# Kernel optimization log

Measured on AMD Instinct MI355X. Metric: run time of the kernel, lower is better.

## Reference

```python
import jax, jax.numpy as jnp
import numpy as np

EPS = 1e-12


def pairwise_sqdist(x, y):
    # x: (B, N, 3), y: (B, M, 3) -> (B, N, M) squared euclidean distances
    xx = jnp.sum(x * x, axis=-1)              # (B, N)
    yy = jnp.sum(y * y, axis=-1)              # (B, M)
    xy = jnp.einsum('bnd,bmd->bnm', x, y)     # (B, N, M)
    d = xx[:, :, None] + yy[None_ if False else yy[:, None, :].shape and 0 or ...] if False else xx[:, :, None] + yy[:, None, :] - 2.0 * xy
    return jnp.maximum(d, 0.0)


def chamfer_l1(x, y):
    # pytorch3d/PoinTr-style ChamferDistanceL1:
    # mean over points of sqrt(min squared dist), averaged over both directions
    d = pairwise_sqdist(x, y)                 # (B, N, M)
    d1 = jnp.min(d, axis=2)                   # (B, N) x -> nearest y
    d2 = jnp.min(d, axis=1)                   # (B, M) y -> nearest x
    d1 = jnp.sqrt(jnp.maximum(d1, EPS))
    d2 = jnp.sqrt(jnp.maximum(d2, EPS))
    return 0.5 * (jnp.mean(d1) + jnp.mean(d2))


def knn1_gather(x, y):
    # For each point in x (B,N,3), find nearest neighbor in y (B,M,3) (K=1)
    # and gather it -> (B, N, 3). Matches knn_points + knn_gather + squeeze.
    d = pairwise_sqdist(x, y)                 # (B, N, M)
    idx = jnp.argmin(d, axis=2)               # (B, N) int
    return jnp.take_along_axis(y, idx[:, :, None], axis=1)  # (B, N, 3)


def volume_with_wedge(p):
    # wedge-product volume over consecutive point triples:
    # V = sum_i (p_i x p_{i+1}) . p_{i+2} / 6  -> (B,)
    c = jnp.cross(p[:, :-2, :], p[:, 1:-1, :])  # (B, N-2, 3)
    return jnp.sum(jnp.einsum('bnd,bnd->bn', c, p[:, 2:, :]), axis=-1) / 6.0


def setup_inputs() -> dict:
    key = jax.random.key(0)
    k1, k2, k3 = jax.random.split(key, 3)
    B, Nc, Nf, M = 2, 512, 8192, 8192
    return {
        'source_coarse': jax.random.normal(k1, (B, Nc, 3), dtype=jnp.float32),
        'source_fine': jax.random.normal(k2, (B, Nf, 3), dtype=jnp.float32),
        'target_points': jax.random.normal(k3, (B, M, 3), dtype=jnp.float32),
    }


def reference(source_coarse, source_fine, target_points):
    lambda_rot = lambda_ref = lambda_align = lambda_geo = 1.0
    B = source_fine.shape[0]
    axis = jnp.broadcast_to(jnp.array([0.0, 0.0, 1.0], dtype=source_fine.dtype), (B, 3))
    plane_normal = jnp.broadcast_to(jnp.array([0.0, 1.0, 0.0], dtype=source_fine.dtype), (B, 3))

    # KNN (K=1) gather of nearest target point for each fine source point
    new_target = knn1_gather(source_fine, target_points)  # (B, Nf, 3)

    # alignment (Chamfer L1) losses
    loss_align_coarse = chamfer_l1(source_coarse, target_points)
    loss_align_fine = chamfer_l1(source_fine, target_points)

    # rotational symmetry loss
    in_proj = jnp.einsum('bij,bj->bi', source_fine, axis)      # (B, Nf)
    re_proj = jnp.einsum('bij,bj->bi', new_target, axis)
    loss_rot = jnp.mean((jnp.linalg.norm(in_proj, axis=-1) - jnp.linalg.norm(re_proj, axis=-1)) ** 2)

    # reflectional symmetry loss
    pn = plane_normal / jnp.linalg.norm(plane_normal, axis=-1, keepdims=True)
    in_dist = jnp.einsum('bij,bj->bi', source_fine, pn)
    re_dist = jnp.einsum('bij,bj->bi', new_target, pn)
    loss_ref = jnp.mean((in_dist - re_dist) ** 2)

    # geometric consistency (wedge-product volume) loss
    loss_geo = jnp.mean((volume_with_wedge(source_fine) - volume_with_wedge(new_target)) ** 2)

    total = (lambda_rot * loss_rot + lambda_ref * loss_ref
             + lambda_align * loss_align_coarse + lambda_align * loss_align_fine
             + lambda_geo * loss_geo)
    return total
```

## Files before the change

### kernel.cpp

```cpp
#include <hip/hip_runtime.h>
#include <stdint.h>
#include <float.h>

using u64 = unsigned long long;
typedef float v2f __attribute__((ext_vector_type(2)));

constexpr int B_ = 2;
constexpr int NC = 512;
constexpr int NF = 8192;
constexpr int MT = 8192;

constexpr int TPB = 256;
constexpr int CF  = 16;
constexpr int TAIL_BLOCKS = 196;

#define DEVINL __device__ __forceinline__

DEVINL v2f pk_mul_vs(v2f a, v2f b){ v2f d; asm("v_pk_mul_f32 %0, %1, %2" : "=v"(d) : "v"(a), "s"(b)); return d; }
DEVINL v2f pk_add_vv(v2f a, v2f b){ v2f d; asm("v_pk_add_f32 %0, %1, %2" : "=v"(d) : "v"(a), "v"(b)); return d; }
DEVINL v2f pk_add_vs(v2f a, v2f b){ v2f d; asm("v_pk_add_f32 %0, %1, %2" : "=v"(d) : "v"(a), "s"(b)); return d; }

__global__ __launch_bounds__(TPB) void prep(
    const float* __restrict__ coarse, const float* __restrict__ fine,
    const float* __restrict__ tgt,
    float* __restrict__ finep, float* __restrict__ tgtp,
    float* __restrict__ coarsep, unsigned* __restrict__ counter)
{
#pragma clang fp contract(off)
    int g = blockIdx.x * TPB + threadIdx.x;
    if (g == 0) *counter = 0;
    if (g < B_ * NF / 2) {
        {
            const float* p = fine + (size_t)g * 6;
            float x0=p[0],y0=p[1],z0=p[2],x1=p[3],y1=p[4],z1=p[5];
            float* o = finep + (size_t)g * 8;
            o[0]=x0; o[1]=x1; o[2]=y0; o[3]=y1; o[4]=z0; o[5]=z1;
            o[6]=(x0*x0+y0*y0)+z0*z0;  o[7]=(x1*x1+y1*y1)+z1*z1;
        }
        {
            const float* p = tgt + (size_t)g * 6;
            float x0=p[0],y0=p[1],z0=p[2],x1=p[3],y1=p[4],z1=p[5];
            float* o = tgtp + (size_t)g * 8;
            o[0]=x0; o[1]=x1; o[2]=y0; o[3]=y1; o[4]=z0; o[5]=z1;
            o[6]=(x0*x0+y0*y0)+z0*z0;  o[7]=(x1*x1+y1*y1)+z1*z1;
        }
        if (g < B_ * NC / 2) {
            const float* p = coarse + (size_t)g * 6;
            float x0=p[0],y0=p[1],z0=p[2],x1=p[3],y1=p[4],z1=p[5];
            float* o = coarsep + (size_t)g * 8;
            o[0]=x0; o[1]=x1; o[2]=y0; o[3]=y1; o[4]=z0; o[5]=z1;
            o[6]=(x0*x0+y0*y0)+z0*z0;  o[7]=(x1*x1+y1*y1)+z1*z1;
        }
    }
}

template<bool ARGMIN>
DEVINL void pairmin_body(const float* __restrict__ P, const v2f* __restrict__ Qp,
                         int nP, int nQpairsB, int b, int row_base,
                         int jp0, int jplen, int chunk, int nRowsTot,
                         u64* __restrict__ outPack, unsigned* __restrict__ outVal)
{
#pragma clang fp contract(off)
    const int tid = threadIdx.x;
    const int row = row_base + tid;
    const float* p = P + ((size_t)b * nP + row) * 3;
    float a0 = p[0], a1 = p[1], a2 = p[2];
    v2f vax = {-2.0f * a0, -2.0f * a0};
    v2f vay = {-2.0f * a1, -2.0f * a1};
    v2f vaz = {-2.0f * a2, -2.0f * a2};
    float xx = (a0*a0 + a1*a1) + a2*a2;
    v2f vxx = {xx, xx};
    float db0 = FLT_MAX, db1 = FLT_MAX;
    int jb0 = 0, jb1 = 0;

    const v2f* Q = Qp + ((size_t)b * nQpairsB + jp0) * 4;
    v2f qx = Q[0], qy = Q[1], qz = Q[2], qw = Q[3];
    int j = jp0 * 2;
    for (int k = 0; k < jplen; ++k) {
        const v2f* Qn = Q + (size_t)(k + 1) * 4;
        v2f nx = Qn[0], ny = Qn[1], nz = Qn[2], nw = Qn[3];
        v2f m0  = pk_mul_vs(vax, qx);
        v2f m1  = pk_mul_vs(vay, qy);
        v2f m2  = pk_mul_vs(vaz, qz);
        v2f s01 = pk_add_vv(m0, m1);
        v2f sxy = pk_add_vv(s01, m2);
        v2f tt  = pk_add_vs(vxx, qw);
        v2f d   = pk_add_vv(tt, sxy);
        if (ARGMIN) {
            float c0 = fmaxf(d.x, 0.0f);
            float c1 = fmaxf(d.y, 0.0f);
            bool t0 = c0 < db0;  db0 = t0 ? c0 : db0;  jb0 = t0 ? j     : jb0;
            bool t1 = c1 < db1;  db1 = t1 ? c1 : db1;  jb1 = t1 ? (j+1) : jb1;
        } else {
            db0 = __builtin_amdgcn_fmed3f(d.x, 0.0f, db0);
            db1 = __builtin_amdgcn_fmed3f(d.y, 0.0f, db1);
        }
        qx = nx; qy = ny; qz = nz; qw = nw;
        j += 2;
    }
    const size_t o = (size_t)chunk * nRowsTot + (size_t)b * nP + row;
    if (ARGMIN) {
        bool odd = (db1 < db0) || (db1 == db0 && jb1 < jb0);
        float db = odd ? db1 : db0;
        int   jb = odd ? jb1 : jb0;
        outPack[o] = ((u64)__float_as_uint(db) << 32) | (unsigned)jb;
    } else {
        outVal[o] = __float_as_uint(fminf(db0, db1));
    }
}

__global__ __launch_bounds__(TPB, 8) void pairmin_all(
    const float* __restrict__ coarse, const float* __restrict__ fine,
    const float* __restrict__ tgt,
    const v2f* __restrict__ finep, const v2f* __restrict__ tgtp,
    const v2f* __restrict__ coarsep,
    u64* __restrict__ pfr, unsigned* __restrict__ pfc,
    unsigned* __restrict__ pcr, unsigned* __restrict__ pcc)
{
    const int bx = blockIdx.x;
    if (bx < 1024) {
        int chunk = bx & 15, yb = (bx >> 4) & 31, b = bx >> 9;
        pairmin_body<false>(tgt, finep, MT, NF/2, b, yb*TPB, chunk*256, 256,
                            chunk, B_*MT, nullptr, pfc);
    } else if (bx < 2048) {
        int i = bx - 1024;
        int chunk = i & 15, yb = (i >> 4) & 31, b = i >> 9;
        pairmin_body<true>(fine, tgtp, NF, MT/2, b, yb*TPB, chunk*256, 256,
                           chunk, B_*NF, pfr, nullptr);
    } else if (bx < 2112) {
        int i = bx - 2048;
        int chunk = i & 15, yb = (i >> 4) & 1, b = i >> 5;
        pairmin_body<false>(coarse, tgtp, NC, MT/2, b, yb*TPB, chunk*256, 256,
                            chunk, B_*NC, nullptr, pcr);
    } else {
        int i = bx - 2112;
        int yb = i & 31, b = i >> 5;
        pairmin_body<false>(tgt, coarsep, MT, NC/2, b, yb*TPB, 0, 256,
                            0, B_*MT, nullptr, pcc);
    }
}

__global__ __launch_bounds__(TPB) void tail_all(
    const float* __restrict__ fine, const float* __restrict__ tgt,
    const u64* __restrict__ pfr, const unsigned* __restrict__ pfc,
    const unsigned* __restrict__ pcr, const unsigned* __restrict__ pcc,
    double* __restrict__ bs, unsigned* __restrict__ counter,
    float* __restrict__ out)
{
    __shared__ float sp[TPB + 2][3], yp[TPB + 2][3];
    __shared__ double redw[4][9];
    __shared__ double lred[4][13];
    __shared__ int lastflag;
    const int bx = blockIdx.x, tid = threadIdx.x;
    const int wave = tid >> 6, lane = tid & 63;

    double v_s = 0, v_d2f = 0, v_d1c = 0, v_d2c = 0, v_yd2 = 0, v_zs = 0, v_zt = 0;
    double vs = 0, vt = 0;
    int role_b = 0;

    if (bx < 64) {
        const int base = bx * TPB;
        const int g = base + tid;
        const int b = base >> 13;  role_b = b;
        u64 best = pfr[g];
        #pragma unroll
        for (int c = 1; c < CF; ++c) {
            u64 p = pfr[(size_t)c * (B_ * NF) + g];
            best = p < best ? p : best;
        }
        float d1 = __uint_as_float((unsigned)(best >> 32));
        int idx  = (int)(best & 0xffffffffULL);
        float s = sqrtf(fmaxf(d1, 1e-12f));
        const float* y  = tgt  + ((size_t)b * MT + idx) * 3;
        const float* sr = fine + (size_t)g * 3;
        float y0 = y[0],  y1 = y[1],  y2 = y[2];
        float s0 = sr[0], s1 = sr[1], s2 = sr[2];
        yp[tid][0] = y0; yp[tid][1] = y1; yp[tid][2] = y2;
        sp[tid][0] = s0; sp[tid][1] = s1; sp[tid][2] = s2;
        const int base_b = base & (NF - 1);
        if (tid < 2 && base_b + TPB + tid < NF) {
            int g2 = base + TPB + tid;
            u64 b2 = pfr[g2];
            #pragma unroll
            for (int c = 1; c < CF; ++c) {
                u64 p = pfr[(size_t)c * (B_ * NF) + g2];
                b2 = p < b2 ? p : b2;
            }
            int i2 = (int)(b2 & 0xffffffffULL);
            const float* yh = tgt  + ((size_t)b * MT + i2) * 3;
            const float* sh = fine + (size_t)g2 * 3;
            #pragma unroll
            for (int k = 0; k < 3; ++k) { yp[TPB + tid][k] = yh[k]; sp[TPB + tid][k] = sh[k]; }
        }
        __syncthreads();
        v_s = s;
        float yd = s1 - y1;
        v_yd2 = (double)(yd * yd);
        v_zs  = (double)(s2 * s2);
        v_zt  = (double)(y2 * y2);
        int rb = base_b + tid;
        if (rb <= NF - 3) {
            {
                const float* a = sp[tid]; const float* c = sp[tid+1]; const float* e = sp[tid+2];
                float c0 = a[1]*c[2] - a[2]*c[1];
                float c1 = a[2]*c[0] - a[0]*c[2];
                float c2 = a[0]*c[1] - a[1]*c[0];
                vs = (double)(c0*e[0] + c1*e[1] + c2*e[2]);
            }
            {
                const float* a = yp[tid]; const float* c = yp[tid+1]; const float* e = yp[tid+2];
                float c0 = a[1]*c[2] - a[2]*c[1];
                float c1 = a[2]*c[0] - a[0]*c[2];
                float c2 = a[0]*c[1] - a[1]*c[0];
                vt = (double)(c0*e[0] + c1*e[1] + c2*e[2]);
            }
        }
    } else if (bx < 128) {
        const int g = (bx - 64) * TPB + tid;
        unsigned best = pfc[g];
        #pragma unroll
        for (int c = 1; c < CF; ++c) best = min(best, pfc[(size_t)c * (B_ * MT) + g]);
        v_d2f = (double)sqrtf(fmaxf(__uint_as_float(best), 1e-12f));
    } else if (bx < 132) {
        const int g = (bx - 128) * TPB + tid;
        unsigned best = pcr[g];
        #pragma unroll
        for (int c = 1; c < 16; ++c) best = min(best, pcr[(size_t)c * (B_ * NC) + g]);
        v_d1c = (double)sqrtf(fmaxf(__uint_as_float(best), 1e-12f));
    } else {
        const int g = (bx - 132) * TPB + tid;
        v_d2c = (double)sqrtf(fmaxf(__uint_as_float(pcc[g]), 1e-12f));
    }

    double r9[9] = {v_s, v_d2f, v_d1c, v_d2c, v_yd2, v_zs, v_zt, vs, vt};
    for (int o = 32; o; o >>= 1) {
        #pragma unroll
        for (int k = 0; k < 9; ++k) r9[k] += __shfl_down(r9[k], o);
    }
    if (lane == 0) {
        #pragma unroll
        for (int k = 0; k < 9; ++k) redw[wave][k] = r9[k];
    }
    __syncthreads();
    if (tid == 0) {
        double t9[9];
        #pragma unroll
        for (int k = 0; k < 9; ++k)
            t9[k] = redw[0][k] + redw[1][k] + redw[2][k] + redw[3][k];
        double* o = bs + (size_t)bx * 16;
        #pragma unroll
        for (int k = 0; k < 16; ++k) o[k] = 0.0;
        o[0] = t9[0]; o[1] = t9[1]; o[2] = t9[2]; o[3] = t9[3]; o[4] = t9[4];
        o[5 + role_b]  = t9[5];
        o[7 + role_b]  = t9[6];
        o[9 + role_b]  = t9[7];
        o[11 + role_b] = t9[8];
        __threadfence();
        unsigned old = atomicAdd(counter, 1u);
        lastflag = (old == TAIL_BLOCKS - 1);
    }
    __syncthreads();
    if (!lastflag) return;

    __threadfence();
    double c13[13];
    if (tid < TAIL_BLOCKS) {
        const double* p = bs + (size_t)tid * 16;
        #pragma unroll
        for (int k = 0; k < 13; ++k) c13[k] = p[k];
    } else {
        #pragma unroll
        for (int k = 0; k < 13; ++k) c13[k] = 0.0;
    }
    for (int o = 32; o; o >>= 1) {
        #pragma unroll
        for (int k = 0; k < 13; ++k) c13[k] += __shfl_down(c13[k], o);
    }
    if (lane == 0) {
        #pragma unroll
        for (int k = 0; k < 13; ++k) lred[wave][k] = c13[k];
    }
    __syncthreads();
    if (tid == 0) {
        double S[13];
        #pragma unroll
        for (int k = 0; k < 13; ++k)
            S[k] = lred[0][k] + lred[1][k] + lred[2][k] + lred[3][k];
        double m_d1f = S[0] / (double)(B_ * NF);
        double m_d2f = S[1] / (double)(B_ * MT);
        double m_d1c = S[2] / (double)(B_ * NC);
        double m_d2c = S[3] / (double)(B_ * MT);
        double loss_align_fine   = 0.5 * (m_d1f + m_d2f);
        double loss_align_coarse = 0.5 * (m_d1c + m_d2c);
        double loss_ref = S[4] / (double)(B_ * NF);
        double loss_rot = 0.0, loss_geo = 0.0;
        for (int b = 0; b < B_; ++b) {
            double dn = sqrt(S[5 + b]) - sqrt(S[7 + b]);
            loss_rot += dn * dn;
            double dv = (S[9 + b] - S[11 + b]) / 6.0;
            loss_geo += dv * dv;
        }
        loss_rot /= (double)B_;
        loss_geo /= (double)B_;
        out[0] = (float)(loss_rot + loss_ref + loss_align_coarse + loss_align_fine + loss_geo);
    }
}

extern "C" void kernel_launch(void* const* d_in, const int* in_sizes, int n_in,
                              void* d_out, int out_size, void* d_ws, size_t ws_size,
                              hipStream_t stream)
{
    const float* src_coarse = (const float*)d_in[0];
    const float* src_fine   = (const float*)d_in[1];
    const float* tgt        = (const float*)d_in[2];
    float* out = (float*)d_out;
    char*  ws  = (char*)d_ws;

    u64*      pfr     = (u64*)(ws);
    unsigned* pfc     = (unsigned*)(ws + 2097152);
    unsigned* pcr     = (unsigned*)(ws + 3145728);
    unsigned* pcc     = (unsigned*)(ws + 3211264);
    float*    finep   = (float*)(ws + 3276800);
    float*    tgtp    = (float*)(ws + 3538944);
    float*    coarsep = (float*)(ws + 3801088);
    double*   bs      = (double*)(ws + 3817472);
    unsigned* counter = (unsigned*)(ws + 3842560);

    prep<<<dim3(32), TPB, 0, stream>>>(src_coarse, src_fine, tgt,
                                       finep, tgtp, coarsep, counter);
    pairmin_all<<<dim3(2176), TPB, 0, stream>>>(
        src_coarse, src_fine, tgt,
        (const v2f*)finep, (const v2f*)tgtp, (const v2f*)coarsep,
        pfr, pfc, pcr, pcc);
    tail_all<<<dim3(TAIL_BLOCKS), TPB, 0, stream>>>(
        src_fine, tgt, pfr, pfc, pcr, pcc, bs, counter, out);
}
```

Before: 132.8 us.

## Register-block two query rows per thread in pairwise min kernel

Each thread now processes two source rows instead of one. Every scalar-loaded pair of target points is reused for both rows, which halves the per-row cost of scalar loads and loop overhead. The grid for the pairwise-min kernel is halved to match, and the loads of the next point pair move two pairs ahead to fit the rotation. The trade-off is more registers per thread and fewer waves, which can leave SIMDs unevenly loaded at the end of the grid.

```diff
diff --git a/kernel.cpp b/kernel.cpp
--- a/kernel.cpp
+++ b/kernel.cpp
@@ -61,51 +61,71 @@
                          u64* __restrict__ outPack, unsigned* __restrict__ outVal)
 {
 #pragma clang fp contract(off)
-    const int tid = threadIdx.x;
-    const int row = row_base + tid;
-    const float* p = P + ((size_t)b * nP + row) * 3;
-    float a0 = p[0], a1 = p[1], a2 = p[2];
-    v2f vax = {-2.0f * a0, -2.0f * a0};
-    v2f vay = {-2.0f * a1, -2.0f * a1};
-    v2f vaz = {-2.0f * a2, -2.0f * a2};
-    float xx = (a0*a0 + a1*a1) + a2*a2;
-    v2f vxx = {xx, xx};
+    const int tid  = threadIdx.x;
+    const int row0 = row_base + tid;
+    const int row1 = row_base + tid + TPB;
+    const float* p0 = P + ((size_t)b * nP + row0) * 3;
+    const float* p1 = P + ((size_t)b * nP + row1) * 3;
+    float a0 = p0[0], a1 = p0[1], a2 = p0[2];
+    float e0 = p1[0], e1 = p1[1], e2 = p1[2];
+    v2f r0x = {-2.0f*a0, -2.0f*a0}, r0y = {-2.0f*a1, -2.0f*a1}, r0z = {-2.0f*a2, -2.0f*a2};
+    v2f r1x = {-2.0f*e0, -2.0f*e0}, r1y = {-2.0f*e1, -2.0f*e1}, r1z = {-2.0f*e2, -2.0f*e2};
+    float xx0 = (a0*a0 + a1*a1) + a2*a2;
+    float xx1 = (e0*e0 + e1*e1) + e2*e2;
+    v2f v0xx = {xx0, xx0}, v1xx = {xx1, xx1};
     float db0 = FLT_MAX, db1 = FLT_MAX;
-    int jb0 = 0, jb1 = 0;
+    float dc0 = FLT_MAX, dc1 = FLT_MAX;
+    int jb0 = 0, jb1 = 0, jc0 = 0, jc1 = 0;
 
     const v2f* Q = Qp + ((size_t)b * nQpairsB + jp0) * 4;
-    v2f qx = Q[0], qy = Q[1], qz = Q[2], qw = Q[3];
+    v2f q0x = Q[0], q0y = Q[1], q0z = Q[2], q0w = Q[3];
+    v2f q1x = Q[4], q1y = Q[5], q1z = Q[6], q1w = Q[7];
     int j = jp0 * 2;
     for (int k = 0; k < jplen; ++k) {
-        const v2f* Qn = Q + (size_t)(k + 1) * 4;
+        const v2f* Qn = Q + (size_t)(k + 2) * 4;
         v2f nx = Qn[0], ny = Qn[1], nz = Qn[2], nw = Qn[3];
-        v2f m0  = pk_mul_vs(vax, qx);
-        v2f m1  = pk_mul_vs(vay, qy);
-        v2f m2  = pk_mul_vs(vaz, qz);
+        v2f m0  = pk_mul_vs(r0x, q0x);
+        v2f m1  = pk_mul_vs(r0y, q0y);
+        v2f m2  = pk_mul_vs(r0z, q0z);
         v2f s01 = pk_add_vv(m0, m1);
         v2f sxy = pk_add_vv(s01, m2);
-        v2f tt  = pk_add_vs(vxx, qw);
-        v2f d   = pk_add_vv(tt, sxy);
+        v2f tt  = pk_add_vs(v0xx, q0w);
+        v2f d0  = pk_add_vv(tt, sxy);
+        v2f n0  = pk_mul_vs(r1x, q0x);
+        v2f n1  = pk_mul_vs(r1y, q0y);
+        v2f n2  = pk_mul_vs(r1z, q0z);
+        v2f t01 = pk_add_vv(n0, n1);
+        v2f txy = pk_add_vv(t01, n2);
+        v2f uu  = pk_add_vs(v1xx, q0w);
+        v2f d1  = pk_add_vv(uu, txy);
         if (ARGMIN) {
-            float c0 = fmaxf(d.x, 0.0f);
-            float c1 = fmaxf(d.y, 0.0f);
+            float c0 = fmaxf(d0.x, 0.0f), c1 = fmaxf(d0.y, 0.0f);
             bool t0 = c0 < db0;  db0 = t0 ? c0 : db0;  jb0 = t0 ? j     : jb0;
             bool t1 = c1 < db1;  db1 = t1 ? c1 : db1;  jb1 = t1 ? (j+1) : jb1;
+            float g0 = fmaxf(d1.x, 0.0f), g1 = fmaxf(d1.y, 0.0f);
+            bool u0 = g0 < dc0;  dc0 = u0 ? g0 : dc0;  jc0 = u0 ? j     : jc0;
+            bool u1 = g1 < dc1;  dc1 = u1 ? g1 : dc1;  jc1 = u1 ? (j+1) : jc1;
         } else {
-            db0 = __builtin_amdgcn_fmed3f(d.x, 0.0f, db0);
-            db1 = __builtin_amdgcn_fmed3f(d.y, 0.0f, db1);
-        }
-        qx = nx; qy = ny; qz = nz; qw = nw;
+            db0 = __builtin_amdgcn_fmed3f(d0.x, 0.0f, db0);
+            db1 = __builtin_amdgcn_fmed3f(d0.y, 0.0f, db1);
+            dc0 = __builtin_amdgcn_fmed3f(d1.x, 0.0f, dc0);
+            dc1 = __builtin_amdgcn_fmed3f(d1.y, 0.0f, dc1);
+        }
+        q0x = q1x; q0y = q1y; q0z = q1z; q0w = q1w;
+        q1x = nx;  q1y = ny;  q1z = nz;  q1w = nw;
         j += 2;
     }
-    const size_t o = (size_t)chunk * nRowsTot + (size_t)b * nP + row;
+    const size_t o0 = (size_t)chunk * nRowsTot + (size_t)b * nP;
     if (ARGMIN) {
-        bool odd = (db1 < db0) || (db1 == db0 && jb1 < jb0);
-        float db = odd ? db1 : db0;
-        int   jb = odd ? jb1 : jb0;
-        outPack[o] = ((u64)__float_as_uint(db) << 32) | (unsigned)jb;
+        bool o1 = (db1 < db0) || (db1 == db0 && jb1 < jb0);
+        float dA = o1 ? db1 : db0;  int jA = o1 ? jb1 : jb0;
+        bool o2 = (dc1 < dc0) || (dc1 == dc0 && jc1 < jc0);
+        float dB = o2 ? dc1 : dc0;  int jB = o2 ? jc1 : jc0;
+        outPack[o0 + row0] = ((u64)__float_as_uint(dA) << 32) | (unsigned)jA;
+        outPack[o0 + row1] = ((u64)__float_as_uint(dB) << 32) | (unsigned)jB;
     } else {
-        outVal[o] = __float_as_uint(fminf(db0, db1));
+        outVal[o0 + row0] = __float_as_uint(fminf(db0, db1));
+        outVal[o0 + row1] = __float_as_uint(fminf(dc0, dc1));
     }
 }
 
@@ -118,24 +138,24 @@
     unsigned* __restrict__ pcr, unsigned* __restrict__ pcc)
 {
     const int bx = blockIdx.x;
-    if (bx < 1024) {
-        int chunk = bx & 15, yb = (bx >> 4) & 31, b = bx >> 9;
-        pairmin_body<false>(tgt, finep, MT, NF/2, b, yb*TPB, chunk*256, 256,
+    if (bx < 512) {
+        int chunk = bx & 15, yb = (bx >> 4) & 15, b = bx >> 8;
+        pairmin_body<false>(tgt, finep, MT, NF/2, b, yb*512, chunk*256, 256,
                             chunk, B_*MT, nullptr, pfc);
-    } else if (bx < 2048) {
+    } else if (bx < 1024) {
+        int i = bx - 512;
+        int chunk = i & 15, yb = (i >> 4) & 15, b = i >> 8;
+        pairmin_body<true>(fine, tgtp, NF, MT/2, b, yb*512, chunk*256, 256,
+                           chunk, B_*NF, pfr, nullptr);
+    } else if (bx < 1056) {
         int i = bx - 1024;
-        int chunk = i & 15, yb = (i >> 4) & 31, b = i >> 9;
-        pairmin_body<true>(fine, tgtp, NF, MT/2, b, yb*TPB, chunk*256, 256,
-                           chunk, B_*NF, pfr, nullptr);
-    } else if (bx < 2112) {
-        int i = bx - 2048;
-        int chunk = i & 15, yb = (i >> 4) & 1, b = i >> 5;
-        pairmin_body<false>(coarse, tgtp, NC, MT/2, b, yb*TPB, chunk*256, 256,
+        int chunk = i & 15, b = i >> 4;
+        pairmin_body<false>(coarse, tgtp, NC, MT/2, b, 0, chunk*256, 256,
                             chunk, B_*NC, nullptr, pcr);
     } else {
-        int i = bx - 2112;
-        int yb = i & 31, b = i >> 5;
-        pairmin_body<false>(tgt, coarsep, MT, NC/2, b, yb*TPB, 0, 256,
+        int i = bx - 1056;
+        int yb = i & 15, b = i >> 4;
+        pairmin_body<false>(tgt, coarsep, MT, NC/2, b, yb*512, 0, 256,
                             0, B_*MT, nullptr, pcc);
     }
 }
@@ -328,7 +348,7 @@
 
     prep<<<dim3(32), TPB, 0, stream>>>(src_coarse, src_fine, tgt,
                                        finep, tgtp, coarsep, counter);
-    pairmin_all<<<dim3(2176), TPB, 0, stream>>>(
+    pairmin_all<<<dim3(1088), TPB, 0, stream>>>(
         src_coarse, src_fine, tgt,
         (const v2f*)finep, (const v2f*)tgtp, (const v2f*)coarsep,
         pfr, pfc, pcr, pcc);
```

Measured after the change: 148.9 us. 12.1% more time.

## Replace brute-force fine/target nearest-neighbor search with uniform grid search

Applied to the files above, without the earlier changes.

Builds a 24^3 uniform spatial grid (counting sort per point set) for target and fine clouds, then answers fine->target argmin and target->fine min queries by expanding shell search with an early-exit bound instead of scanning all 8192 points. This removes the O(N*M) brute-force pass for the two large directions and the 16-way chunk reduction in the tail. It adds sorting overhead, per-thread divergent irregular loops, and fewer blocks; the grid bounds and margin assume roughly normal-distributed inputs, though correctness holds via clamped cells and the radius bound.

```diff
diff --git a/kernel.cpp b/kernel.cpp
--- a/kernel.cpp
+++ b/kernel.cpp
@@ -1,6 +1,7 @@
 #include <hip/hip_runtime.h>
 #include <stdint.h>
 #include <float.h>
+#include <math.h>
 
 using u64 = unsigned long long;
 typedef float v2f __attribute__((ext_vector_type(2)));
@@ -14,68 +15,203 @@
 constexpr int CF  = 16;
 constexpr int TAIL_BLOCKS = 196;
 
+constexpr int   G    = 24;
+constexpr int   G3   = G * G * G;
+constexpr int   G3P  = 14336;
+constexpr float GO   = -3.0f;
+constexpr float GH   = 0.25f;
+constexpr float GINVH= 4.0f;
+constexpr float MARGIN = 1e-3f;
+
 #define DEVINL __device__ __forceinline__
+
+DEVINL float fmulrn(float a, float b){ return __fmul_rn(a,b); }
+DEVINL float faddrn(float a, float b){ return __fadd_rn(a,b); }
+DEVINL float fsubrn(float a, float b){ return __fsub_rn(a,b); }
 
 DEVINL v2f pk_mul_vs(v2f a, v2f b){ v2f d; asm("v_pk_mul_f32 %0, %1, %2" : "=v"(d) : "v"(a), "s"(b)); return d; }
 DEVINL v2f pk_add_vv(v2f a, v2f b){ v2f d; asm("v_pk_add_f32 %0, %1, %2" : "=v"(d) : "v"(a), "v"(b)); return d; }
 DEVINL v2f pk_add_vs(v2f a, v2f b){ v2f d; asm("v_pk_add_f32 %0, %1, %2" : "=v"(d) : "v"(a), "s"(b)); return d; }
 
-__global__ __launch_bounds__(TPB) void prep(
+DEVINL int cell_of(float c){
+    int v = (int)floorf((c - GO) * GINVH);
+    return min(max(v, 0), G - 1);
+}
+
+__global__ __launch_bounds__(1024) void prep_build(
     const float* __restrict__ coarse, const float* __restrict__ fine,
     const float* __restrict__ tgt,
-    float* __restrict__ finep, float* __restrict__ tgtp,
-    float* __restrict__ coarsep, unsigned* __restrict__ counter)
+    float4* __restrict__ spts, int* __restrict__ sjall, int* __restrict__ ofsall,
+    int* __restrict__ pcell,
+    float* __restrict__ tgtp, float* __restrict__ coarsep,
+    unsigned* __restrict__ counter)
 {
 #pragma clang fp contract(off)
-    int g = blockIdx.x * TPB + threadIdx.x;
-    if (g == 0) *counter = 0;
-    if (g < B_ * NF / 2) {
+    const int bx = blockIdx.x, tid = threadIdx.x;
+    if (bx >= 4) {
+        int idx = (bx - 4) * 1024 + tid;
+        if (idx == 0) *counter = 0;
         {
-            const float* p = fine + (size_t)g * 6;
+            const float* p = tgt + (size_t)idx * 6;
             float x0=p[0],y0=p[1],z0=p[2],x1=p[3],y1=p[4],z1=p[5];
-            float* o = finep + (size_t)g * 8;
+            float* o = tgtp + (size_t)idx * 8;
             o[0]=x0; o[1]=x1; o[2]=y0; o[3]=y1; o[4]=z0; o[5]=z1;
             o[6]=(x0*x0+y0*y0)+z0*z0;  o[7]=(x1*x1+y1*y1)+z1*z1;
         }
-        {
-            const float* p = tgt + (size_t)g * 6;
+        if (idx < B_ * NC / 2) {
+            const float* p = coarse + (size_t)idx * 6;
             float x0=p[0],y0=p[1],z0=p[2],x1=p[3],y1=p[4],z1=p[5];
-            float* o = tgtp + (size_t)g * 8;
+            float* o = coarsep + (size_t)idx * 8;
             o[0]=x0; o[1]=x1; o[2]=y0; o[3]=y1; o[4]=z0; o[5]=z1;
             o[6]=(x0*x0+y0*y0)+z0*z0;  o[7]=(x1*x1+y1*y1)+z1*z1;
         }
-        if (g < B_ * NC / 2) {
-            const float* p = coarse + (size_t)g * 6;
-            float x0=p[0],y0=p[1],z0=p[2],x1=p[3],y1=p[4],z1=p[5];
-            float* o = coarsep + (size_t)g * 8;
-            o[0]=x0; o[1]=x1; o[2]=y0; o[3]=y1; o[4]=z0; o[5]=z1;
-            o[6]=(x0*x0+y0*y0)+z0*z0;  o[7]=(x1*x1+y1*y1)+z1*z1;
-        }
+        return;
+    }
+
+    __shared__ int cnt[G3P];
+    __shared__ int wsum[16];
+    const int set = bx;
+    const float* pts = (set < 2 ? tgt : fine) + (size_t)(set & 1) * 8192 * 3;
+    float4* sp = spts  + (size_t)set * 8192;
+    int*    sj = sjall + (size_t)set * 8192;
+    int*    of = ofsall + (size_t)set * (G3 + 1);
+    int*    pc = pcell + (size_t)set * 8192;
+
+    for (int i = tid; i < G3P; i += 1024) cnt[i] = 0;
+    __syncthreads();
+    for (int i = tid; i < 8192; i += 1024) {
+        const float* p = pts + (size_t)i * 3;
+        int c = (cell_of(p[0]) * G + cell_of(p[1])) * G + cell_of(p[2]);
+        pc[i] = c;
+        atomicAdd(&cnt[c], 1);
+    }
+    __syncthreads();
+    const int lane = tid & 63, wid = tid >> 6;
+    const int base = tid * 14;
+    int loc[14]; int s = 0;
+    #pragma unroll
+    for (int k = 0; k < 14; ++k) { loc[k] = s; s += cnt[base + k]; }
+    int v = s;
+    for (int o = 1; o < 64; o <<= 1) { int t = __shfl_up(v, o); if (lane >= o) v += t; }
+    if (lane == 63) wsum[wid] = v;
+    __syncthreads();
+    if (wid == 0 && lane < 16) {
+        int w = wsum[lane];
+        for (int o = 1; o < 16; o <<= 1) { int t = __shfl_up(w, o); if (lane >= o) w += t; }
+        wsum[lane] = w;
+    }
+    __syncthreads();
+    int excl = ((wid == 0) ? 0 : wsum[wid - 1]) + (v - s);
+    #pragma unroll
+    for (int k = 0; k < 14; ++k) {
+        int c = base + k;
+        int st = excl + loc[k];
+        if (c < G3) of[c] = st;
+        cnt[c] = st;
+    }
+    if (tid == 0) of[G3] = 8192;
+    __syncthreads();
+    for (int i = tid; i < 8192; i += 1024) {
+        int c = pc[i];
+        int dst = atomicAdd(&cnt[c], 1);
+        const float* p = pts + (size_t)i * 3;
+        float a = p[0], b = p[1], cc = p[2];
+        sp[dst] = make_float4(a, b, cc,
+                              faddrn(faddrn(fmulrn(a,a), fmulrn(b,b)), fmulrn(cc,cc)));
+        sj[dst] = i;
     }
 }
 
 template<bool ARGMIN>
-DEVINL void pairmin_body(const float* __restrict__ P, const v2f* __restrict__ Qp,
-                         int nP, int nQpairsB, int b, int row_base,
-                         int jp0, int jplen, int chunk, int nRowsTot,
-                         u64* __restrict__ outPack, unsigned* __restrict__ outVal)
+DEVINL u64 grid_nn(float q0, float q1, float q2,
+                   const float4* __restrict__ sp, const int* __restrict__ sj,
+                   const int* __restrict__ ofs)
+{
+    float xx = faddrn(faddrn(fmulrn(q0,q0), fmulrn(q1,q1)), fmulrn(q2,q2));
+    const int cx = cell_of(q0), cy = cell_of(q1), cz = cell_of(q2);
+    u64 best = ~0ull;
+    float bestf = FLT_MAX;
+
+    auto scan_cell = [&](int x, int y, int z) {
+        int c = (x * G + y) * G + z;
+        int s = ofs[c], e = ofs[c + 1];
+        int k = s;
+        for (; k + 4 <= e; k += 4) {
+            float4 p0 = sp[k], p1 = sp[k+1], p2 = sp[k+2], p3 = sp[k+3];
+            int j0=0, j1=0, j2=0, j3=0;
+            if (ARGMIN) { j0 = sj[k]; j1 = sj[k+1]; j2 = sj[k+2]; j3 = sj[k+3]; }
+            float4 ps[4] = {p0, p1, p2, p3};
+            int    js[4] = {j0, j1, j2, j3};
+            #pragma unroll
+            for (int u = 0; u < 4; ++u) {
+                float4 p = ps[u];
+                float xy = faddrn(faddrn(fmulrn(q0,p.x), fmulrn(q1,p.y)), fmulrn(q2,p.z));
+                float t  = faddrn(xx, p.w);
+                float d  = fsubrn(t, fmulrn(2.0f, xy));
+                d = fmaxf(d, 0.0f);
+                if (ARGMIN) {
+                    u64 pk = ((u64)__float_as_uint(d) << 32) | (unsigned)js[u];
+                    best = pk < best ? pk : best;
+                }
+                bestf = fminf(bestf, d);
+            }
+        }
+        for (; k < e; ++k) {
+            float4 p = sp[k];
+            float xy = faddrn(faddrn(fmulrn(q0,p.x), fmulrn(q1,p.y)), fmulrn(q2,p.z));
+            float t  = faddrn(xx, p.w);
+            float d  = fsubrn(t, fmulrn(2.0f, xy));
+            d = fmaxf(d, 0.0f);
+            if (ARGMIN) {
+                u64 pk = ((u64)__float_as_uint(d) << 32) | (unsigned)sj[k];
+                best = pk < best ? pk : best;
+            }
+            bestf = fminf(bestf, d);
+        }
+    };
+
+    for (int r = 0; r < G; ++r) {
+        if (r >= 2) {
+            float rb = (float)(r - 1) * GH;
+            if (bestf + MARGIN <= rb * rb) break;
+        }
+        int xlo = max(cx - r, 0), xhi = min(cx + r, G - 1);
+        int ylo = max(cy - r, 0), yhi = min(cy + r, G - 1);
+        int zlo = max(cz - r, 0), zhi = min(cz + r, G - 1);
+        for (int x = xlo; x <= xhi; ++x) {
+            bool xe = (x == cx - r) || (x == cx + r);
+            for (int y = ylo; y <= yhi; ++y) {
+                bool face = xe || (y == cy - r) || (y == cy + r);
+                if (face) {
+                    for (int z = zlo; z <= zhi; ++z) scan_cell(x, y, z);
+                } else {
+                    if (cz - r >= 0)     scan_cell(x, y, cz - r);
+                    if (cz + r <= G - 1) scan_cell(x, y, cz + r);
+                }
+            }
+        }
+    }
+    if (ARGMIN) return best;
+    return (u64)__float_as_uint(bestf);
+}
+
+DEVINL void pairmin_val(const float* __restrict__ P, const v2f* __restrict__ Qp,
+                        int nP, int nQpairsB, int b, int row_base,
+                        int jp0, int jplen, int chunk, int nRowsTot,
+                        unsigned* __restrict__ outVal)
 {
 #pragma clang fp contract(off)
     const int tid = threadIdx.x;
     const int row = row_base + tid;
     const float* p = P + ((size_t)b * nP + row) * 3;
     float a0 = p[0], a1 = p[1], a2 = p[2];
-    v2f vax = {-2.0f * a0, -2.0f * a0};
-    v2f vay = {-2.0f * a1, -2.0f * a1};
-    v2f vaz = {-2.0f * a2, -2.0f * a2};
+    v2f vax = {-2.0f*a0, -2.0f*a0}, vay = {-2.0f*a1, -2.0f*a1}, vaz = {-2.0f*a2, -2.0f*a2};
     float xx = (a0*a0 + a1*a1) + a2*a2;
     v2f vxx = {xx, xx};
     float db0 = FLT_MAX, db1 = FLT_MAX;
-    int jb0 = 0, jb1 = 0;
 
     const v2f* Q = Qp + ((size_t)b * nQpairsB + jp0) * 4;
     v2f qx = Q[0], qy = Q[1], qz = Q[2], qw = Q[3];
-    int j = jp0 * 2;
     for (int k = 0; k < jplen; ++k) {
         const v2f* Qn = Q + (size_t)(k + 1) * 4;
         v2f nx = Qn[0], ny = Qn[1], nz = Qn[2], nw = Qn[3];
@@ -86,57 +222,50 @@
         v2f sxy = pk_add_vv(s01, m2);
         v2f tt  = pk_add_vs(vxx, qw);
         v2f d   = pk_add_vv(tt, sxy);
-        if (ARGMIN) {
-            float c0 = fmaxf(d.x, 0.0f);
-            float c1 = fmaxf(d.y, 0.0f);
-            bool t0 = c0 < db0;  db0 = t0 ? c0 : db0;  jb0 = t0 ? j     : jb0;
-            bool t1 = c1 < db1;  db1 = t1 ? c1 : db1;  jb1 = t1 ? (j+1) : jb1;
-        } else {
-            db0 = __builtin_amdgcn_fmed3f(d.x, 0.0f, db0);
-            db1 = __builtin_amdgcn_fmed3f(d.y, 0.0f, db1);
-        }
+        db0 = __builtin_amdgcn_fmed3f(d.x, 0.0f, db0);
+        db1 = __builtin_amdgcn_fmed3f(d.y, 0.0f, db1);
         qx = nx; qy = ny; qz = nz; qw = nw;
-        j += 2;
-    }
-    const size_t o = (size_t)chunk * nRowsTot + (size_t)b * nP + row;
-    if (ARGMIN) {
-        bool odd = (db1 < db0) || (db1 == db0 && jb1 < jb0);
-        float db = odd ? db1 : db0;
-        int   jb = odd ? jb1 : jb0;
-        outPack[o] = ((u64)__float_as_uint(db) << 32) | (unsigned)jb;
-    } else {
-        outVal[o] = __float_as_uint(fminf(db0, db1));
-    }
-}
-
-__global__ __launch_bounds__(TPB, 8) void pairmin_all(
+    }
+    outVal[(size_t)chunk * nRowsTot + (size_t)b * nP + row] =
+        __float_as_uint(fminf(db0, db1));
+}
+
+__global__ __launch_bounds__(TPB) void pair_all(
     const float* __restrict__ coarse, const float* __restrict__ fine,
     const float* __restrict__ tgt,
-    const v2f* __restrict__ finep, const v2f* __restrict__ tgtp,
-    const v2f* __restrict__ coarsep,
+    const float4* __restrict__ spts, const int* __restrict__ sjall,
+    const int* __restrict__ ofsall,
+    const v2f* __restrict__ tgtp, const v2f* __restrict__ coarsep,
     u64* __restrict__ pfr, unsigned* __restrict__ pfc,
     unsigned* __restrict__ pcr, unsigned* __restrict__ pcc)
 {
-    const int bx = blockIdx.x;
-    if (bx < 1024) {
-        int chunk = bx & 15, yb = (bx >> 4) & 31, b = bx >> 9;
-        pairmin_body<false>(tgt, finep, MT, NF/2, b, yb*TPB, chunk*256, 256,
-                            chunk, B_*MT, nullptr, pfc);
-    } else if (bx < 2048) {
-        int i = bx - 1024;
-        int chunk = i & 15, yb = (i >> 4) & 31, b = i >> 9;
-        pairmin_body<true>(fine, tgtp, NF, MT/2, b, yb*TPB, chunk*256, 256,
-                           chunk, B_*NF, pfr, nullptr);
-    } else if (bx < 2112) {
-        int i = bx - 2048;
+    const int bx = blockIdx.x, tid = threadIdx.x;
+    if (bx < 64) {
+        int g = bx * TPB + tid;
+        int b = g >> 13;
+        const float* q = fine + (size_t)g * 3;
+        pfr[g] = grid_nn<true>(q[0], q[1], q[2],
+                               spts + (size_t)b * 8192, sjall + (size_t)b * 8192,
+                               ofsall + (size_t)b * (G3 + 1));
+    } else if (bx < 128) {
+        int g = (bx - 64) * TPB + tid;
+        int b = g >> 13;
+        const float* q = tgt + (size_t)g * 3;
+        int set = 2 + b;
+        u64 r = grid_nn<false>(q[0], q[1], q[2],
+                               spts + (size_t)set * 8192, sjall + (size_t)set * 8192,
+                               ofsall + (size_t)set * (G3 + 1));
+        pfc[g] = (unsigned)r;
+    } else if (bx < 192) {
+        int i = bx - 128;
         int chunk = i & 15, yb = (i >> 4) & 1, b = i >> 5;
-        pairmin_body<false>(coarse, tgtp, NC, MT/2, b, yb*TPB, chunk*256, 256,
-                            chunk, B_*NC, nullptr, pcr);
+        pairmin_val(coarse, tgtp, NC, MT/2, b, yb*TPB, chunk*256, 256,
+                    chunk, B_*NC, pcr);
     } else {
-        int i = bx - 2112;
+        int i = bx - 192;
         int yb = i & 31, b = i >> 5;
-        pairmin_body<false>(tgt, coarsep, MT, NC/2, b, yb*TPB, 0, 256,
-                            0, B_*MT, nullptr, pcc);
+        pairmin_val(tgt, coarsep, MT, NC/2, b, yb*TPB, 0, 256,
+                    0, B_*MT, pcc);
     }
 }
 
@@ -163,11 +292,6 @@
         const int g = base + tid;
         const int b = base >> 13;  role_b = b;
         u64 best = pfr[g];
-        #pragma unroll
-        for (int c = 1; c < CF; ++c) {
-            u64 p = pfr[(size_t)c * (B_ * NF) + g];
-            best = p < best ? p : best;
-        }
         float d1 = __uint_as_float((unsigned)(best >> 32));
         int idx  = (int)(best & 0xffffffffULL);
         float s = sqrtf(fmaxf(d1, 1e-12f));
@@ -181,11 +305,6 @@
         if (tid < 2 && base_b + TPB + tid < NF) {
             int g2 = base + TPB + tid;
             u64 b2 = pfr[g2];
-            #pragma unroll
-            for (int c = 1; c < CF; ++c) {
-                u64 p = pfr[(size_t)c * (B_ * NF) + g2];
-                b2 = p < b2 ? p : b2;
-            }
             int i2 = (int)(b2 & 0xffffffffULL);
             const float* yh = tgt  + ((size_t)b * MT + i2) * 3;
             const float* sh = fine + (size_t)g2 * 3;
@@ -217,15 +336,12 @@
         }
     } else if (bx < 128) {
         const int g = (bx - 64) * TPB + tid;
-        unsigned best = pfc[g];
-        #pragma unroll
-        for (int c = 1; c < CF; ++c) best = min(best, pfc[(size_t)c * (B_ * MT) + g]);
-        v_d2f = (double)sqrtf(fmaxf(__uint_as_float(best), 1e-12f));
+        v_d2f = (double)sqrtf(fmaxf(__uint_as_float(pfc[g]), 1e-12f));
     } else if (bx < 132) {
         const int g = (bx - 128) * TPB + tid;
         unsigned best = pcr[g];
         #pragma unroll
-        for (int c = 1; c < 16; ++c) best = min(best, pcr[(size_t)c * (B_ * NC) + g]);
+        for (int c = 1; c < CF; ++c) best = min(best, pcr[(size_t)c * (B_ * NC) + g]);
         v_d1c = (double)sqrtf(fmaxf(__uint_as_float(best), 1e-12f));
     } else {
         const int g = (bx - 132) * TPB + tid;
@@ -317,21 +433,24 @@
     char*  ws  = (char*)d_ws;
 
     u64*      pfr     = (u64*)(ws);
-    unsigned* pfc     = (unsigned*)(ws + 2097152);
-    unsigned* pcr     = (unsigned*)(ws + 3145728);
-    unsigned* pcc     = (unsigned*)(ws + 3211264);
-    float*    finep   = (float*)(ws + 3276800);
-    float*    tgtp    = (float*)(ws + 3538944);
-    float*    coarsep = (float*)(ws + 3801088);
-    double*   bs      = (double*)(ws + 3817472);
-    unsigned* counter = (unsigned*)(ws + 3842560);
-
-    prep<<<dim3(32), TPB, 0, stream>>>(src_coarse, src_fine, tgt,
-                                       finep, tgtp, coarsep, counter);
-    pairmin_all<<<dim3(2176), TPB, 0, stream>>>(
-        src_coarse, src_fine, tgt,
-        (const v2f*)finep, (const v2f*)tgtp, (const v2f*)coarsep,
-        pfr, pfc, pcr, pcc);
+    unsigned* pfc     = (unsigned*)(ws + 131072);
+    unsigned* pcr     = (unsigned*)(ws + 196608);
+    unsigned* pcc     = (unsigned*)(ws + 262144);
+    float*    tgtp    = (float*)(ws + 327680);
+    float*    coarsep = (float*)(ws + 589824);
+    float4*   spts    = (float4*)(ws + 606208);
+    int*      sjall   = (int*)(ws + 1130496);
+    int*      ofsall  = (int*)(ws + 1261568);
+    int*      pcell   = (int*)(ws + 1482768);
+    double*   bs      = (double*)(ws + 1613840);
+    unsigned* counter = (unsigned*)(ws + 1638928);
+
+    prep_build<<<dim3(12), 1024, 0, stream>>>(
+        src_coarse, src_fine, tgt, spts, sjall, ofsall, pcell,
+        tgtp, coarsep, counter);
+    pair_all<<<dim3(256), TPB, 0, stream>>>(
+        src_coarse, src_fine, tgt, spts, sjall, ofsall,
+        (const v2f*)tgtp, (const v2f*)coarsep, pfr, pfc, pcr, pcc);
     tail_all<<<dim3(TAIL_BLOCKS), TPB, 0, stream>>>(
         src_fine, tgt, pfr, pfc, pcr, pcc, bs, counter, out);
 }
```

Measured after the change: 392.2 us. 2.95x slower.
